# Optimization experiments

Hardware: AMD Instinct MI355X
Metric: run time of the kernel (lower is better)

The kernel has to match this reference:

```python
import jax, jax.numpy as jnp
import numpy as np

N_NODES = 50000
N_EDGES = 800000
D_IN = 64
D_OUT = 64


def setup_inputs() -> dict:
    key = jax.random.key(0)
    ks = jax.random.split(key, 5)
    feat = jax.random.normal(ks[0], (N_NODES, D_IN), dtype=jnp.float32)
    src = jax.random.randint(ks[1], (N_EDGES,), 0, N_NODES, dtype=jnp.int64)
    dst = jax.random.randint(ks[2], (N_EDGES,), 0, N_NODES, dtype=jnp.int64)
    # Xavier-uniform-ish scale for weights
    lim = float(np.sqrt(6.0 / (D_IN + D_OUT)) * np.sqrt(2.0))
    W_neigh = jax.random.uniform(ks[3], (D_OUT, D_IN), dtype=jnp.float32, minval=-lim, maxval=lim)
    W_self = jax.random.uniform(ks[4], (D_OUT, D_IN), dtype=jnp.float32, minval=-lim, maxval=lim)
    b_self = jnp.zeros((D_OUT,), dtype=jnp.float32)
    return {"feat": feat, "src": src, "dst": dst,
            "W_neigh": W_neigh, "W_self": W_self, "b_self": b_self}


def reference(feat, src, dst, W_neigh, W_self, b_self):
    # srcdata = fc_neigh(feat_src)  -> [N, D_OUT]
    srcdata = feat @ W_neigh.T
    # A_div.T @ srcdata == mean of transformed source feats over in-edges per dst.
    # deg[j] = A.sum(0)[j]; column scaling by 1/deg then transpose-SpMM.
    agg = jax.ops.segment_sum(srcdata[src], dst, num_segments=N_NODES)  # [N, D_OUT]
    deg = jax.ops.segment_sum(jnp.ones_like(dst, dtype=srcdata.dtype), dst,
                              num_segments=N_NODES)  # [N]
    # Zero-degree columns stay zero in the sparse product (no stored nonzeros).
    dstdata = jnp.where(deg[:, None] > 0, agg / jnp.maximum(deg, 1.0)[:, None], 0.0)
    # rst = fc_self(feat_dst) + dstdata ; feat_dst = feat[:N_dst] = feat (square A)
    return feat @ W_self.T + b_self + dstdata
```

## Files before the change

### kernel.cpp

```cpp
#include <hip/hip_runtime.h>

#define N_NODES 50000
#define N_EDGES 800000
#define D 64
#define RB 128
#define NBUCK 391
#define CAP 3072
#define PAD 16
#define NFEATBLK 3125
#define GN 64

typedef __attribute__((ext_vector_type(8))) __bf16 bf16x8;
typedef __attribute__((ext_vector_type(4))) float f32x4;
typedef __attribute__((ext_vector_type(2))) float f32x2;

__device__ inline unsigned f2bf(float f) {
    unsigned b = __builtin_bit_cast(unsigned, f);
    b += 0x7fffu + ((b >> 16) & 1u);
    return b >> 16;
}

__device__ inline void acc16(float* acc, uint4 v) {
    f32x2 a;
    a = __builtin_amdgcn_cvt_pk_f32_fp8((int)v.x, false); acc[0]  += a.x; acc[1]  += a.y;
    a = __builtin_amdgcn_cvt_pk_f32_fp8((int)v.x, true);  acc[2]  += a.x; acc[3]  += a.y;
    a = __builtin_amdgcn_cvt_pk_f32_fp8((int)v.y, false); acc[4]  += a.x; acc[5]  += a.y;
    a = __builtin_amdgcn_cvt_pk_f32_fp8((int)v.y, true);  acc[6]  += a.x; acc[7]  += a.y;
    a = __builtin_amdgcn_cvt_pk_f32_fp8((int)v.z, false); acc[8]  += a.x; acc[9]  += a.y;
    a = __builtin_amdgcn_cvt_pk_f32_fp8((int)v.z, true);  acc[10] += a.x; acc[11] += a.y;
    a = __builtin_amdgcn_cvt_pk_f32_fp8((int)v.w, false); acc[12] += a.x; acc[13] += a.y;
    a = __builtin_amdgcn_cvt_pk_f32_fp8((int)v.w, true);  acc[14] += a.x; acc[15] += a.y;
}

__global__ __launch_bounds__(256) void pre_kernel(const float* __restrict__ feat,
                                                  const float* __restrict__ Wn,
                                                  const float* __restrict__ Ws,
                                                  unsigned short* __restrict__ fb,
                                                  unsigned* __restrict__ fq,
                                                  unsigned short* __restrict__ wnb,
                                                  unsigned short* __restrict__ wsb) {
    int b = blockIdx.x;
    int t = threadIdx.x;
    if (b < NFEATBLK) {
        int i = b * 256 + t;
        float4 v = ((const float4*)feat)[i];
        uint2 o;
        o.x = f2bf(v.x) | (f2bf(v.y) << 16);
        o.y = f2bf(v.z) | (f2bf(v.w) << 16);
        ((uint2*)fb)[i] = o;
        int q = __builtin_amdgcn_cvt_pk_fp8_f32(v.x, v.y, 0, false);
        q = __builtin_amdgcn_cvt_pk_fp8_f32(v.z, v.w, q, true);
        fq[i] = (unsigned)q;
    } else {
        for (int i = t; i < D * D; i += 256) {
            wnb[i] = (unsigned short)f2bf(Wn[i]);
            wsb[i] = (unsigned short)f2bf(Ws[i]);
        }
    }
}

__global__ __launch_bounds__(1024) void passB_kernel(const int* __restrict__ src, const int* __restrict__ dst,
                                                     int* __restrict__ bcursor, unsigned int* __restrict__ ebuf) {
    __shared__ int cnt[NBUCK];
    __shared__ int base[NBUCK];
    int t = threadIdx.x;
    for (int i = t; i < NBUCK; i += 1024) cnt[i] = 0;
    __syncthreads();
    int eb = blockIdx.x * 8192;
    int s_[8], b_[8], dl_[8];
#pragma unroll
    for (int k = 0; k < 8; ++k) {
        int e = eb + k * 1024 + t;
        if (e < N_EDGES) {
            int dv = dst[e];
            s_[k] = src[e];
            b_[k] = dv >> 7;
            dl_[k] = dv & (RB - 1);
            atomicAdd(&cnt[b_[k]], 1);
        } else b_[k] = -1;
    }
    __syncthreads();
    for (int i = t; i < NBUCK; i += 1024) {
        int c = cnt[i];
        base[i] = c ? atomicAdd(&bcursor[i * PAD], c) : 0;
    }
    __syncthreads();
#pragma unroll
    for (int k = 0; k < 8; ++k) {
        if (b_[k] >= 0) {
            int pos = atomicAdd(&base[b_[k]], 1);
            if (pos < CAP)
                ebuf[(size_t)b_[k] * CAP + pos] = (unsigned)s_[k] | ((unsigned)dl_[k] << 16);
        }
    }
}

#define ALD 68
__global__ __launch_bounds__(256) void gather_mfma_kernel(
        const unsigned short* __restrict__ fb, const unsigned char* __restrict__ fq,
        const int* __restrict__ bcursor, const unsigned int* __restrict__ ebuf,
        const unsigned short* __restrict__ wsb, const unsigned short* __restrict__ wnb,
        const float* __restrict__ bias, float* __restrict__ out) {
    __shared__ int cnt[RB];
    __shared__ int cur[RB];
    __shared__ int sorted[CAP];
    __shared__ float agg[GN * ALD];
    int t = threadIdx.x;
    int bk = blockIdx.x >> 1;
    int half = blockIdx.x & 1;
    int s0 = bk * CAP;
    int n = bcursor[bk * PAD];
    if (n > CAP) n = CAP;
    if (t < RB) cnt[t] = 0;
    __syncthreads();
    for (int i = t; i < n; i += 256) atomicAdd(&cnt[ebuf[s0 + i] >> 16], 1);
    __syncthreads();
    int c = (t < RB) ? cnt[t] : 0;
    if (t < RB) cur[t] = c;
    __syncthreads();
    for (int d = 1; d < RB; d <<= 1) {
        int v = (t < RB && t >= d) ? cur[t - d] : 0;
        __syncthreads();
        if (t < RB) cur[t] += v;
        __syncthreads();
    }
    if (t < RB) cur[t] -= c;
    __syncthreads();
    for (int i = t; i < n; i += 256) {
        unsigned r = ebuf[s0 + i];
        int p = atomicAdd(&cur[r >> 16], 1);
        sorted[p] = (int)(r & 0xFFFFu);
    }
    __syncthreads();
    int ns = t >> 2, p = t & 3;
    int dl = half * GN + ns;
    int dg = cnt[dl];
    int start = cur[dl] - dg;
    float acc[16];
#pragma unroll
    for (int j = 0; j < 16; ++j) acc[j] = 0.f;
    const unsigned char* fqp = fq + p * 16;
    int i = 0;
    for (; i + 4 <= dg; i += 4) {
        int id0 = sorted[start + i + 0];
        int id1 = sorted[start + i + 1];
        int id2 = sorted[start + i + 2];
        int id3 = sorted[start + i + 3];
        uint4 v0 = *(const uint4*)(fqp + (size_t)id0 * D);
        uint4 v1 = *(const uint4*)(fqp + (size_t)id1 * D);
        uint4 v2 = *(const uint4*)(fqp + (size_t)id2 * D);
        uint4 v3 = *(const uint4*)(fqp + (size_t)id3 * D);
        acc16(acc, v0); acc16(acc, v1); acc16(acc, v2); acc16(acc, v3);
    }
    for (; i < dg; ++i) {
        int id = sorted[start + i];
        uint4 v = *(const uint4*)(fqp + (size_t)id * D);
        acc16(acc, v);
    }
    float inv = (dg > 0) ? 1.0f / (float)dg : 0.f;
#pragma unroll
    for (int j = 0; j < 16; j += 4) {
        float4 o = make_float4(acc[j] * inv, acc[j + 1] * inv, acc[j + 2] * inv, acc[j + 3] * inv);
        *(float4*)(&agg[ns * ALD + p * 16 + j]) = o;
    }
    __syncthreads();
    int r0 = blockIdx.x * GN;
    int w = t >> 6, lane = t & 63;
    int m = lane & 15, quad = lane >> 4;
    int row = r0 + 16 * w + m;
    int rowA = row < N_NODES ? row : N_NODES - 1;
    bf16x8 aS0 = *(const bf16x8*)(fb + (size_t)rowA * D + 0  + quad * 8);
    bf16x8 aS1 = *(const bf16x8*)(fb + (size_t)rowA * D + 32 + quad * 8);
    bf16x8 aA0, aA1;
#pragma unroll
    for (int j = 0; j < 8; ++j) {
        aA0[j] = (__bf16)agg[(16 * w + m) * ALD + 0  + quad * 8 + j];
        aA1[j] = (__bf16)agg[(16 * w + m) * ALD + 32 + quad * 8 + j];
    }
#pragma unroll
    for (int tt = 0; tt < 4; ++tt) {
        int nn = 16 * tt + m;
        bf16x8 bS0 = *(const bf16x8*)(wsb + (size_t)nn * D + 0  + quad * 8);
        bf16x8 bS1 = *(const bf16x8*)(wsb + (size_t)nn * D + 32 + quad * 8);
        bf16x8 bN0 = *(const bf16x8*)(wnb + (size_t)nn * D + 0  + quad * 8);
        bf16x8 bN1 = *(const bf16x8*)(wnb + (size_t)nn * D + 32 + quad * 8);
        f32x4 cc = {0.f, 0.f, 0.f, 0.f};
        cc = __builtin_amdgcn_mfma_f32_16x16x32_bf16(aS0, bS0, cc, 0, 0, 0);
        cc = __builtin_amdgcn_mfma_f32_16x16x32_bf16(aS1, bS1, cc, 0, 0, 0);
        cc = __builtin_amdgcn_mfma_f32_16x16x32_bf16(aA0, bN0, cc, 0, 0, 0);
        cc = __builtin_amdgcn_mfma_f32_16x16x32_bf16(aA1, bN1, cc, 0, 0, 0);
        float bv = bias[16 * tt + m];
#pragma unroll
        for (int reg = 0; reg < 4; ++reg) {
            int orow = r0 + 16 * w + quad * 4 + reg;
            if (orow < N_NODES)
                out[(size_t)orow * D + 16 * tt + m] = cc[reg] + bv;
        }
    }
}

extern "C" void kernel_launch(void* const* d_in, const int* in_sizes, int n_in,
                              void* d_out, int out_size, void* d_ws, size_t ws_size,
                              hipStream_t stream) {
    const float* feat  = (const float*)d_in[0];
    const int*   src   = (const int*)d_in[1];
    const int*   dst   = (const int*)d_in[2];
    const float* Wn    = (const float*)d_in[3];
    const float* Wself = (const float*)d_in[4];
    const float* bself = (const float*)d_in[5];
    float* out = (float*)d_out;

    unsigned short* featb = (unsigned short*)d_ws;
    unsigned*       featq = (unsigned*)(featb + (size_t)N_NODES * D);
    unsigned short* wnb   = (unsigned short*)(featq + (size_t)N_NODES * D / 4);
    unsigned short* wsb   = wnb + D * D;
    unsigned int*   ebuf  = (unsigned int*)(wsb + D * D);
    int* bcursor = (int*)(ebuf + (size_t)NBUCK * CAP);

    hipMemsetAsync(bcursor, 0, (size_t)NBUCK * PAD * sizeof(int), stream);

    pre_kernel<<<NFEATBLK + 1, 256, 0, stream>>>(feat, Wn, Wself, featb, featq, wnb, wsb);
    passB_kernel<<<(N_EDGES + 8191) / 8192, 1024, 0, stream>>>(src, dst, bcursor, ebuf);
    gather_mfma_kernel<<<2 * NBUCK, 256, 0, stream>>>(
        featb, (const unsigned char*)featq, bcursor, ebuf, wsb, wnb, bself, out);
}
```

Before: 114.3 us.

## Fuse preprocessing, bucketing and gather into one cooperative kernel with grid syncs

Replaces the memset plus three separate kernel launches with a single cooperative kernel that converts features and weights, buckets edges by destination, then gathers and runs the MFMA projection, separated by grid-wide barriers. This is meant to remove launch gaps and the memset. In exchange, each phase now runs on a fixed grid of 782 blocks: the bucketing phase uses 196 blocks of 256 threads instead of larger blocks, and grid.sync adds barrier cost. The old multi-kernel path is kept as a fallback if the cooperative launch fails, and the fallback now zeroes the cursors inside pre_kernel.

```diff
diff --git a/kernel.cpp b/kernel.cpp
--- a/kernel.cpp
+++ b/kernel.cpp
@@ -1,4 +1,7 @@
 #include <hip/hip_runtime.h>
+#include <hip/hip_cooperative_groups.h>
+
+namespace cg = cooperative_groups;
 
 #define N_NODES 50000
 #define N_EDGES 800000
@@ -9,6 +12,11 @@
 #define PAD 16
 #define NFEATBLK 3125
 #define GN 64
+#define NBLK 782
+#define NTHREAD 256
+#define NCHUNK 196
+#define CHUNK 4096
+#define ALD 68
 
 typedef __attribute__((ext_vector_type(8))) __bf16 bf16x8;
 typedef __attribute__((ext_vector_type(4))) float f32x4;
@@ -32,13 +40,172 @@
     a = __builtin_amdgcn_cvt_pk_f32_fp8((int)v.w, true);  acc[14] += a.x; acc[15] += a.y;
 }
 
+__global__ __launch_bounds__(256, 4) void fused_kernel(
+        const float* __restrict__ feat, const int* __restrict__ src, const int* __restrict__ dst,
+        const float* __restrict__ Wn, const float* __restrict__ Ws, const float* __restrict__ bias,
+        unsigned short* __restrict__ fb, unsigned* __restrict__ fq,
+        unsigned short* __restrict__ wnb, unsigned short* __restrict__ wsb,
+        unsigned int* __restrict__ ebuf, int* __restrict__ bcursor, float* __restrict__ out) {
+    __shared__ int cnt[RB];
+    __shared__ int cur[RB];
+    __shared__ int sorted[CAP];
+    __shared__ float agg[GN * ALD];
+    cg::grid_group grid = cg::this_grid();
+    int t = threadIdx.x;
+    int b = blockIdx.x;
+    int gid = b * NTHREAD + t;
+
+    for (int i = gid; i < NBUCK * PAD; i += NBLK * NTHREAD) bcursor[i] = 0;
+    for (int i = gid; i < N_NODES * D / 4; i += NBLK * NTHREAD) {
+        float4 v = ((const float4*)feat)[i];
+        uint2 o;
+        o.x = f2bf(v.x) | (f2bf(v.y) << 16);
+        o.y = f2bf(v.z) | (f2bf(v.w) << 16);
+        ((uint2*)fb)[i] = o;
+        int q = __builtin_amdgcn_cvt_pk_fp8_f32(v.x, v.y, 0, false);
+        q = __builtin_amdgcn_cvt_pk_fp8_f32(v.z, v.w, q, true);
+        fq[i] = (unsigned)q;
+    }
+    if (b == NBLK - 1) {
+        for (int i = t; i < D * D; i += NTHREAD) {
+            wnb[i] = (unsigned short)f2bf(Wn[i]);
+            wsb[i] = (unsigned short)f2bf(Ws[i]);
+        }
+    }
+    grid.sync();
+
+    if (b < NCHUNK) {
+        int* cntB  = sorted;
+        int* baseB = sorted + NBUCK;
+        for (int i = t; i < NBUCK; i += NTHREAD) cntB[i] = 0;
+        __syncthreads();
+        int e0 = b * CHUNK;
+#pragma unroll
+        for (int k = 0; k < CHUNK / NTHREAD; ++k) {
+            int e = e0 + k * NTHREAD + t;
+            if (e < N_EDGES) atomicAdd(&cntB[dst[e] >> 7], 1);
+        }
+        __syncthreads();
+        for (int i = t; i < NBUCK; i += NTHREAD) {
+            int c = cntB[i];
+            baseB[i] = c ? atomicAdd(&bcursor[i * PAD], c) : 0;
+        }
+        __syncthreads();
+#pragma unroll
+        for (int k = 0; k < CHUNK / NTHREAD; ++k) {
+            int e = e0 + k * NTHREAD + t;
+            if (e < N_EDGES) {
+                int dv = dst[e];
+                int bk = dv >> 7, dl = dv & (RB - 1);
+                int pos = atomicAdd(&baseB[bk], 1);
+                if (pos < CAP)
+                    ebuf[(size_t)bk * CAP + pos] = (unsigned)src[e] | ((unsigned)dl << 16);
+            }
+        }
+    }
+    grid.sync();
+
+    int bk = b >> 1;
+    int half = b & 1;
+    int s0 = bk * CAP;
+    int n = bcursor[bk * PAD];
+    if (n > CAP) n = CAP;
+    if (t < RB) cnt[t] = 0;
+    __syncthreads();
+    for (int i = t; i < n; i += NTHREAD) atomicAdd(&cnt[ebuf[s0 + i] >> 16], 1);
+    __syncthreads();
+    int c = (t < RB) ? cnt[t] : 0;
+    if (t < RB) cur[t] = c;
+    __syncthreads();
+    for (int d = 1; d < RB; d <<= 1) {
+        int v = (t < RB && t >= d) ? cur[t - d] : 0;
+        __syncthreads();
+        if (t < RB) cur[t] += v;
+        __syncthreads();
+    }
+    if (t < RB) cur[t] -= c;
+    __syncthreads();
+    for (int i = t; i < n; i += NTHREAD) {
+        unsigned r = ebuf[s0 + i];
+        int p = atomicAdd(&cur[r >> 16], 1);
+        sorted[p] = (int)(r & 0xFFFFu);
+    }
+    __syncthreads();
+    int ns = t >> 2, p = t & 3;
+    int dl = half * GN + ns;
+    int dg = cnt[dl];
+    int start = cur[dl] - dg;
+    float acc[16];
+#pragma unroll
+    for (int j = 0; j < 16; ++j) acc[j] = 0.f;
+    const unsigned char* fqp = (const unsigned char*)fq + p * 16;
+    int i = 0;
+    for (; i + 4 <= dg; i += 4) {
+        int id0 = sorted[start + i + 0];
+        int id1 = sorted[start + i + 1];
+        int id2 = sorted[start + i + 2];
+        int id3 = sorted[start + i + 3];
+        uint4 v0 = *(const uint4*)(fqp + (size_t)id0 * D);
+        uint4 v1 = *(const uint4*)(fqp + (size_t)id1 * D);
+        uint4 v2 = *(const uint4*)(fqp + (size_t)id2 * D);
+        uint4 v3 = *(const uint4*)(fqp + (size_t)id3 * D);
+        acc16(acc, v0); acc16(acc, v1); acc16(acc, v2); acc16(acc, v3);
+    }
+    for (; i < dg; ++i) {
+        int id = sorted[start + i];
+        uint4 v = *(const uint4*)(fqp + (size_t)id * D);
+        acc16(acc, v);
+    }
+    float inv = (dg > 0) ? 1.0f / (float)dg : 0.f;
+#pragma unroll
+    for (int j = 0; j < 16; j += 4) {
+        float4 o = make_float4(acc[j] * inv, acc[j + 1] * inv, acc[j + 2] * inv, acc[j + 3] * inv);
+        *(float4*)(&agg[ns * ALD + p * 16 + j]) = o;
+    }
+    __syncthreads();
+    int r0 = b * GN;
+    int w = t >> 6, lane = t & 63;
+    int m = lane & 15, quad = lane >> 4;
+    int row = r0 + 16 * w + m;
+    int rowA = row < N_NODES ? row : N_NODES - 1;
+    bf16x8 aS0 = *(const bf16x8*)(fb + (size_t)rowA * D + 0  + quad * 8);
+    bf16x8 aS1 = *(const bf16x8*)(fb + (size_t)rowA * D + 32 + quad * 8);
+    bf16x8 aA0, aA1;
+#pragma unroll
+    for (int j = 0; j < 8; ++j) {
+        aA0[j] = (__bf16)agg[(16 * w + m) * ALD + 0  + quad * 8 + j];
+        aA1[j] = (__bf16)agg[(16 * w + m) * ALD + 32 + quad * 8 + j];
+    }
+#pragma unroll
+    for (int tt = 0; tt < 4; ++tt) {
+        int nn = 16 * tt + m;
+        bf16x8 bS0 = *(const bf16x8*)(wsb + (size_t)nn * D + 0  + quad * 8);
+        bf16x8 bS1 = *(const bf16x8*)(wsb + (size_t)nn * D + 32 + quad * 8);
+        bf16x8 bN0 = *(const bf16x8*)(wnb + (size_t)nn * D + 0  + quad * 8);
+        bf16x8 bN1 = *(const bf16x8*)(wnb + (size_t)nn * D + 32 + quad * 8);
+        f32x4 cc = {0.f, 0.f, 0.f, 0.f};
+        cc = __builtin_amdgcn_mfma_f32_16x16x32_bf16(aS0, bS0, cc, 0, 0, 0);
+        cc = __builtin_amdgcn_mfma_f32_16x16x32_bf16(aS1, bS1, cc, 0, 0, 0);
+        cc = __builtin_amdgcn_mfma_f32_16x16x32_bf16(aA0, bN0, cc, 0, 0, 0);
+        cc = __builtin_amdgcn_mfma_f32_16x16x32_bf16(aA1, bN1, cc, 0, 0, 0);
+        float bv = bias[16 * tt + m];
+#pragma unroll
+        for (int reg = 0; reg < 4; ++reg) {
+            int orow = r0 + 16 * w + quad * 4 + reg;
+            if (orow < N_NODES)
+                out[(size_t)orow * D + 16 * tt + m] = cc[reg] + bv;
+        }
+    }
+}
+
 __global__ __launch_bounds__(256) void pre_kernel(const float* __restrict__ feat,
                                                   const float* __restrict__ Wn,
                                                   const float* __restrict__ Ws,
                                                   unsigned short* __restrict__ fb,
                                                   unsigned* __restrict__ fq,
                                                   unsigned short* __restrict__ wnb,
-                                                  unsigned short* __restrict__ wsb) {
+                                                  unsigned short* __restrict__ wsb,
+                                                  int* __restrict__ bcursor) {
     int b = blockIdx.x;
     int t = threadIdx.x;
     if (b < NFEATBLK) {
@@ -56,6 +223,7 @@
             wnb[i] = (unsigned short)f2bf(Wn[i]);
             wsb[i] = (unsigned short)f2bf(Ws[i]);
         }
+        for (int i = t; i < NBUCK * PAD; i += 256) bcursor[i] = 0;
     }
 }
 
@@ -95,7 +263,6 @@
     }
 }
 
-#define ALD 68
 __global__ __launch_bounds__(256) void gather_mfma_kernel(
         const unsigned short* __restrict__ fb, const unsigned char* __restrict__ fq,
         const int* __restrict__ bcursor, const unsigned int* __restrict__ ebuf,
@@ -217,10 +384,15 @@
     unsigned int*   ebuf  = (unsigned int*)(wsb + D * D);
     int* bcursor = (int*)(ebuf + (size_t)NBUCK * CAP);
 
-    hipMemsetAsync(bcursor, 0, (size_t)NBUCK * PAD * sizeof(int), stream);
-
-    pre_kernel<<<NFEATBLK + 1, 256, 0, stream>>>(feat, Wn, Wself, featb, featq, wnb, wsb);
-    passB_kernel<<<(N_EDGES + 8191) / 8192, 1024, 0, stream>>>(src, dst, bcursor, ebuf);
-    gather_mfma_kernel<<<2 * NBUCK, 256, 0, stream>>>(
-        featb, (const unsigned char*)featq, bcursor, ebuf, wsb, wnb, bself, out);
-}
+    void* args[] = {(void*)&feat, (void*)&src, (void*)&dst, (void*)&Wn, (void*)&Wself,
+                    (void*)&bself, (void*)&featb, (void*)&featq, (void*)&wnb, (void*)&wsb,
+                    (void*)&ebuf, (void*)&bcursor, (void*)&out};
+    hipError_t err = hipLaunchCooperativeKernel((const void*)fused_kernel,
+                                                dim3(NBLK), dim3(NTHREAD), args, 0, stream);
+    if (err != hipSuccess) {
+        pre_kernel<<<NFEATBLK + 1, 256, 0, stream>>>(feat, Wn, Wself, featb, featq, wnb, wsb, bcursor);
+        passB_kernel<<<(N_EDGES + 8191) / 8192, 1024, 0, stream>>>(src, dst, bcursor, ebuf);
+        gather_mfma_kernel<<<2 * NBUCK, 256, 0, stream>>>(
+            featb, (const unsigned char*)featq, bcursor, ebuf, wsb, wnb, bself, out);
+    }
+}
```

Result: slower. 278.8 us (+143.9%).
